# Optimization experiments

Hardware: AMD Instinct MI355X
Metric: run time of the kernel (lower is better)

The kernel has to match this reference:

```python
import jax, jax.numpy as jnp
import numpy as np

NUM_HEADS = 16
TEMPERATURE = 1.0


def setup_inputs() -> dict:
    key = jax.random.key(0)
    ks = jax.random.split(key, 6)
    B, H = 2048, 2048
    return {
        "hidden_states": jax.random.normal(ks[0], (B, H), dtype=jnp.float32),
        "attention_mask": jnp.ones((B,), dtype=bool),
        "Wq": jax.random.normal(ks[1], (H, H), dtype=jnp.float32) * 0.02,
        "Wk": jax.random.normal(ks[2], (H, H), dtype=jnp.float32) * 0.02,
        "Wv": jax.random.normal(ks[3], (H, H), dtype=jnp.float32) * 0.02,
        "Wo": jax.random.normal(ks[4], (H, H), dtype=jnp.float32) * 0.02,
        "scale_param": jnp.full((1,), -3.0, dtype=jnp.float32),
    }


def reference(hidden_states, attention_mask, Wq, Wk, Wv, Wo, scale_param):
    B, H = hidden_states.shape
    nh = NUM_HEADS
    hd = H // nh
    # projections (torch Linear: x @ W.T), reshape to [heads, batch, head_dim]
    q = (hidden_states @ Wq.T).reshape(B, nh, hd).transpose(1, 0, 2)
    k = (hidden_states @ Wk.T).reshape(B, nh, hd).transpose(1, 0, 2)
    v = (hidden_states @ Wv.T).reshape(B, nh, hd).transpose(1, 0, 2)
    # cross-batch scores [heads, B, B]
    scores = jnp.einsum('hqd,hkd->hqk', q, k) / (hd ** 0.5 * TEMPERATURE)
    neg_inf = jnp.float32(-jnp.inf)
    eye = jnp.eye(B, dtype=bool)  # exclude self-attention (diagonal)
    scores = jnp.where(eye[None, :, :], neg_inf, scores)
    scores = jnp.where(attention_mask[None, None, :], scores, neg_inf)
    attn = jax.nn.softmax(scores, axis=-1)
    attn = jnp.nan_to_num(attn, nan=0.0)  # rows fully masked -> 0 (dropout=0 is identity)
    ctx = jnp.einsum('hqk,hkd->hqd', attn, v)  # [heads, B, head_dim]
    ctx = ctx.transpose(1, 0, 2).reshape(B, H)
    cross = ctx @ Wo.T
    scale = jax.nn.sigmoid(scale_param[0])
    return hidden_states + scale * cross
```

## Files before the change

### kernel.cpp

```cpp
#include <hip/hip_runtime.h>

typedef __bf16 bf16;
typedef __attribute__((ext_vector_type(8))) __bf16 bf16x8;
typedef __attribute__((ext_vector_type(4))) float f32x4;
typedef __attribute__((ext_vector_type(4))) short s16x4;

#define HDIM 2048

__device__ __forceinline__ void glds16(const void* g, void* l) {
  __builtin_amdgcn_global_load_lds((const __attribute__((address_space(1))) void*)g,
                                   (__attribute__((address_space(3))) void*)l,
                                   16, 0, 0);
}

#define MFMA16(a, b, c) __builtin_amdgcn_mfma_f32_16x16x32_bf16(a, b, c, 0, 0, 0)

__global__ __launch_bounds__(256) void cvt5(
    const float* __restrict__ s0, const float* __restrict__ s1,
    const float* __restrict__ s2, const float* __restrict__ s3,
    const float* __restrict__ s4,
    bf16* __restrict__ d0, bf16* __restrict__ d1, bf16* __restrict__ d2,
    bf16* __restrict__ d3, bf16* __restrict__ d4) {
  const float* s; bf16* d;
  switch (blockIdx.y) {
    case 0: s = s0; d = d0; break;
    case 1: s = s1; d = d1; break;
    case 2: s = s2; d = d2; break;
    case 3: s = s3; d = d3; break;
    default: s = s4; d = d4; break;
  }
  const size_t base = (size_t)blockIdx.x * 4096 + (threadIdx.x << 2);
  for (int i = 0; i < 4; i++) {
    const float4 v = *(const float4*)(s + base + i * 1024);
    union { bf16 h[4]; s16x4 s4v; } u;
    u.h[0] = (bf16)v.x; u.h[1] = (bf16)v.y; u.h[2] = (bf16)v.z; u.h[3] = (bf16)v.w;
    *(s16x4*)(d + base + i * 1024) = u.s4v;
  }
}

__device__ __forceinline__ void gemm128_core(const bf16* __restrict__ A,
                                             const bf16* __restrict__ B,
                                             int rowBase, int colBase,
                                             f32x4 acc[4][4],
                                             bf16* ldsA, bf16* ldsB) {
  const int t = threadIdx.x;
  const int w = t >> 6, l = t & 63;
  const int wr = (w >> 1) << 6, wc = (w & 1) << 6;
  const int lr = l & 15, lq = l >> 4;

  for (int mi = 0; mi < 4; mi++)
    for (int ni = 0; ni < 4; ni++)
      for (int r = 0; r < 4; r++) acc[mi][ni][r] = 0.f;

  const int sRow = (w << 4) + (l >> 2);
  const int sCol = (l & 3) << 3;
  const bf16* gA = A + (size_t)(rowBase + sRow) * HDIM + sCol;
  const bf16* gB = B + (size_t)(colBase + sRow) * HDIM + sCol;
  bf16* lA = ldsA + (w << 9);
  bf16* lB = ldsB + (w << 9);

  for (int k0 = 0; k0 < HDIM; k0 += 32) {
    glds16(gA, lA);
    glds16(gA + (size_t)64 * HDIM, lA + 2048);
    glds16(gB, lB);
    glds16(gB + (size_t)64 * HDIM, lB + 2048);
    gA += 32; gB += 32;
    __syncthreads();

    bf16x8 af[4], bfr[4];
    for (int mi = 0; mi < 4; mi++)
      af[mi] = *(const bf16x8*)&ldsA[(wr + mi * 16 + lr) * 32 + lq * 8];
    for (int ni = 0; ni < 4; ni++)
      bfr[ni] = *(const bf16x8*)&ldsB[(wc + ni * 16 + lr) * 32 + lq * 8];
    for (int mi = 0; mi < 4; mi++)
      for (int ni = 0; ni < 4; ni++)
        acc[mi][ni] = MFMA16(af[mi], bfr[ni], acc[mi][ni]);
    __syncthreads();
  }
}

__global__ __launch_bounds__(256) void qkv_gemm(
    const bf16* __restrict__ hs, const bf16* __restrict__ Wq,
    const bf16* __restrict__ Wk, const bf16* __restrict__ Wv,
    bf16* __restrict__ qb, bf16* __restrict__ Kf, bf16* __restrict__ Vf) {
  __shared__ bf16 ldsA[128 * 32];
  __shared__ bf16 ldsB[128 * 32];
  const int z = blockIdx.z;
  const bf16* W = (z == 0) ? Wq : (z == 1) ? Wk : Wv;
  const int rowBase = blockIdx.y << 7, colBase = blockIdx.x << 7;
  f32x4 acc[4][4];
  gemm128_core(hs, W, rowBase, colBase, acc, ldsA, ldsB);

  const int t = threadIdx.x;
  const int w = t >> 6, l = t & 63;
  const int wr = (w >> 1) << 6, wc = (w & 1) << 6;
  const int lr = l & 15, lq = l >> 4;

  if (z == 0) {
    for (int mi = 0; mi < 4; mi++)
      for (int ni = 0; ni < 4; ni++) {
        const int col = colBase + wc + ni * 16 + lr;
        const int row0 = rowBase + wr + mi * 16 + lq * 4;
        for (int r = 0; r < 4; r++)
          qb[(size_t)(row0 + r) * HDIM + col] = (bf16)acc[mi][ni][r];
      }
  } else if (z == 1) {
    for (int mi = 0; mi < 4; mi++)
      for (int ni = 0; ni < 4; ni++) {
        const int dim = colBase + wc + ni * 16 + lr;
        const int hh = dim >> 7, ks = (dim >> 5) & 3, kh = (dim >> 3) & 3, j = dim & 7;
        const int row0 = rowBase + wr + mi * 16 + lq * 4;
        for (int r = 0; r < 4; r++) {
          const int key = row0 + r;
          const int kbk = key >> 7, kni = (key >> 4) & 7, kl = key & 15;
          Kf[(((size_t)hh * 16 + kbk) * 32 + kni * 4 + ks) * 512 +
             (kh * 16 + kl) * 8 + j] = (bf16)acc[mi][ni][r];
        }
      }
  } else {
    for (int mi = 0; mi < 4; mi++)
      for (int ni = 0; ni < 4; ni++) {
        const int dim = colBase + wc + ni * 16 + lr;
        const int hh = dim >> 7, vni = (dim >> 4) & 7, ll = dim & 15;
        const int row0 = rowBase + wr + mi * 16 + lq * 4;
        const int kbk = row0 >> 7, ks = (row0 >> 5) & 3, lh = (row0 >> 3) & 3;
        const int j0 = row0 & 7;
        union { bf16 h4[4]; s16x4 v; } u;
        for (int r = 0; r < 4; r++) u.h4[r] = (bf16)acc[mi][ni][r];
        *(s16x4*)&Vf[(((size_t)hh * 16 + kbk) * 32 + vni * 4 + ks) * 512 +
                     (lh * 16 + ll) * 8 + j0] = u.v;
      }
  }
}

__global__ __launch_bounds__(256, 2) void attn_kernel(
    const bf16* __restrict__ qb, const bf16* __restrict__ Kf,
    const bf16* __restrict__ Vf, const unsigned char* __restrict__ amask,
    bf16* __restrict__ ctx) {
  __shared__ bf16 Kl[32 * 512];
  __shared__ bf16 Vl[32 * 512];
  __shared__ bf16 Pl[4 * 16 * 128];

  const int qt = blockIdx.x, h = blockIdx.y;
  const int t = threadIdx.x, w = t >> 6, l = t & 63;
  const int lr = l & 15, lq = l >> 4;
  bf16* Pw = Pl + (w << 11);

  bf16x8 aq[4];
  for (int ks = 0; ks < 4; ks++)
    aq[ks] = *(const bf16x8*)&qb[(size_t)(qt * 64 + w * 16 + lr) * HDIM +
                                 h * 128 + ks * 32 + lq * 8];

  f32x4 o[8];
  for (int ni = 0; ni < 8; ni++)
    for (int r = 0; r < 4; r++) o[ni][r] = 0.f;
  float lsum[4] = {0.f, 0.f, 0.f, 0.f};
  int qrow[4];
  for (int r = 0; r < 4; r++) qrow[r] = qt * 64 + w * 16 + lq * 4 + r;

  const float c = 0.08838834764831845f * 1.4426950408889634f;

  for (int kbk = 0; kbk < 16; kbk++) {
    const size_t tileOff = ((size_t)h * 16 + kbk) * 32 * 512;

    for (int i = 0; i < 8; i++) {
      const int frag = i * 4 + w;
      glds16(Kf + tileOff + frag * 512 + l * 8, Kl + frag * 512);
    }
    bf16x8 vtmp[8];
    for (int i = 0; i < 8; i++) {
      const int frag = i * 4 + w;
      vtmp[i] = *(const bf16x8*)&Vf[tileOff + frag * 512 + l * 8];
    }
    for (int i = 0; i < 8; i++) {
      const int frag = i * 4 + w;
      *(bf16x8*)&Vl[frag * 512 + l * 8] = vtmp[i];
    }
    __syncthreads();

    f32x4 s[8];
    for (int ni = 0; ni < 8; ni++)
      for (int r = 0; r < 4; r++) s[ni][r] = 0.f;
    for (int ks = 0; ks < 4; ks++) {
      bf16x8 bk[8];
      for (int ni = 0; ni < 8; ni++)
        bk[ni] = *(const bf16x8*)&Kl[(ni * 4 + ks) * 512 + l * 8];
      for (int ni = 0; ni < 8; ni++) s[ni] = MFMA16(aq[ks], bk[ni], s[ni]);
    }

    float mk[8];
    for (int ni = 0; ni < 8; ni++)
      mk[ni] = amask[kbk * 128 + ni * 16 + lr] ? 1.f : 0.f;
    const bool diagBlk = (kbk == (qt >> 1));
    for (int ni = 0; ni < 8; ni++) {
      const int col = kbk * 128 + ni * 16 + lr;
      for (int r = 0; r < 4; r++) {
        float p = __builtin_exp2f(s[ni][r] * c) * mk[ni];
        if (diagBlk && col == qrow[r]) p = 0.f;
        s[ni][r] = p;
        lsum[r] += p;
      }
    }

    for (int ni = 0; ni < 8; ni++)
      for (int r = 0; r < 4; r++) {
        const int row = lq * 4 + r;
        Pw[row * 128 + (((ni * 2 + (lr >> 3)) ^ row) << 3) + (lr & 7)] = (bf16)s[ni][r];
      }

    for (int ks = 0; ks < 4; ks++) {
      bf16x8 bv[8];
      for (int ni = 0; ni < 8; ni++)
        bv[ni] = *(const bf16x8*)&Vl[(ni * 4 + ks) * 512 + l * 8];
      const bf16x8 ap = *(const bf16x8*)&Pw[lr * 128 + (((ks * 4 + lq) ^ lr) << 3)];
      for (int ni = 0; ni < 8; ni++) o[ni] = MFMA16(ap, bv[ni], o[ni]);
    }
    __syncthreads();
  }

  for (int r = 0; r < 4; r++)
    for (int off = 1; off < 16; off <<= 1)
      lsum[r] += __shfl_xor(lsum[r], off);

  for (int ni = 0; ni < 8; ni++)
    for (int r = 0; r < 4; r++) {
      const int row = qrow[r];
      const int col = h * 128 + ni * 16 + lr;
      const float li = lsum[r];
      ctx[(size_t)row * HDIM + col] = (bf16)((li > 0.f) ? o[ni][r] / li : 0.f);
    }
}

__global__ __launch_bounds__(256) void out_gemm(
    const bf16* __restrict__ ctx, const bf16* __restrict__ Wo,
    const float* __restrict__ hs, const float* __restrict__ scale_p,
    float* __restrict__ outp) {
  __shared__ bf16 ldsA[128 * 32];
  __shared__ bf16 ldsB[64 * 32];
  const int rowBase = blockIdx.y << 7, colBase = blockIdx.x << 6;
  const int t = threadIdx.x;
  const int w = t >> 6, l = t & 63;
  const int wr = (w >> 1) << 6, wc = (w & 1) << 5;
  const int lr = l & 15, lq = l >> 4;

  f32x4 acc[4][2];
  for (int mi = 0; mi < 4; mi++)
    for (int ni = 0; ni < 2; ni++)
      for (int r = 0; r < 4; r++) acc[mi][ni][r] = 0.f;

  const int sRow = (w << 4) + (l >> 2);
  const int sCol = (l & 3) << 3;
  const bf16* gA = ctx + (size_t)(rowBase + sRow) * HDIM + sCol;
  const bf16* gB = Wo + (size_t)(colBase + sRow) * HDIM + sCol;
  bf16* lA = ldsA + (w << 9);
  bf16* lB = ldsB + (w << 9);

  for (int k0 = 0; k0 < HDIM; k0 += 32) {
    glds16(gA, lA);
    glds16(gA + (size_t)64 * HDIM, lA + 2048);
    glds16(gB, lB);
    gA += 32; gB += 32;
    __syncthreads();

    bf16x8 af[4], bfr[2];
    for (int mi = 0; mi < 4; mi++)
      af[mi] = *(const bf16x8*)&ldsA[(wr + mi * 16 + lr) * 32 + lq * 8];
    for (int ni = 0; ni < 2; ni++)
      bfr[ni] = *(const bf16x8*)&ldsB[(wc + ni * 16 + lr) * 32 + lq * 8];
    for (int mi = 0; mi < 4; mi++)
      for (int ni = 0; ni < 2; ni++)
        acc[mi][ni] = MFMA16(af[mi], bfr[ni], acc[mi][ni]);
    __syncthreads();
  }

  const float sig = 1.0f / (1.0f + __expf(-scale_p[0]));
  for (int mi = 0; mi < 4; mi++)
    for (int ni = 0; ni < 2; ni++) {
      const int col = colBase + wc + ni * 16 + lr;
      const int row0 = rowBase + wr + mi * 16 + lq * 4;
      for (int r = 0; r < 4; r++) {
        const size_t idx = (size_t)(row0 + r) * HDIM + col;
        outp[idx] = hs[idx] + sig * acc[mi][ni][r];
      }
    }
}

extern "C" void kernel_launch(void* const* d_in, const int* in_sizes, int n_in,
                              void* d_out, int out_size, void* d_ws, size_t ws_size,
                              hipStream_t stream) {
  const float* hs = (const float*)d_in[0];
  const unsigned char* amask = (const unsigned char*)d_in[1];
  const float* Wq = (const float*)d_in[2];
  const float* Wk = (const float*)d_in[3];
  const float* Wv = (const float*)d_in[4];
  const float* Wo = (const float*)d_in[5];
  const float* scale_p = (const float*)d_in[6];
  float* outp = (float*)d_out;

  const size_t N = (size_t)HDIM * HDIM;
  bf16* qb   = (bf16*)d_ws;
  bf16* Kf   = qb + N;
  bf16* Vf   = Kf + N;
  bf16* ctx  = Vf + N;
  bf16* hs16 = ctx + N;
  bf16* Wq16 = hs16 + N;
  bf16* Wk16 = Wq16 + N;
  bf16* Wv16 = Wk16 + N;
  bf16* Wo16 = Wv16 + N;

  cvt5<<<dim3(1024, 5), 256, 0, stream>>>(hs, Wq, Wk, Wv, Wo,
                                          hs16, Wq16, Wk16, Wv16, Wo16);
  qkv_gemm<<<dim3(16, 16, 3), 256, 0, stream>>>(hs16, Wq16, Wk16, Wv16, qb, Kf, Vf);
  attn_kernel<<<dim3(32, 16), 256, 0, stream>>>(qb, Kf, Vf, amask, ctx);
  out_gemm<<<dim3(32, 16), 256, 0, stream>>>(ctx, Wo16, hs, scale_p, outp);
}
```

Measured before the change: 278.3 us.

## Split attention keys across waves and use fragment-ordered LDS tiles in GEMMs

The GEMM kernels now stage A/B tiles in LDS in MFMA-fragment order, so each lane reads one contiguous 16-byte chunk and the old row-strided reads that caused bank conflicts go away. The attention kernel reorganises its warps into 2 query groups × 2 key halves. Each wave handles 32 query rows against 64 keys, computing S transposed and reading the mask as a packed word. Partial outputs and row sums are combined through LDS at the end. This raises reuse of K/V fragments per wave, at the cost of an extra cross-wave reduction and the extra synchronisation it needs.

```diff
diff --git a/kernel.cpp b/kernel.cpp
--- a/kernel.cpp
+++ b/kernel.cpp
@@ -45,33 +45,36 @@
                                              bf16* ldsA, bf16* ldsB) {
   const int t = threadIdx.x;
   const int w = t >> 6, l = t & 63;
-  const int wr = (w >> 1) << 6, wc = (w & 1) << 6;
-  const int lr = l & 15, lq = l >> 4;
 
   for (int mi = 0; mi < 4; mi++)
     for (int ni = 0; ni < 4; ni++)
       for (int r = 0; r < 4; r++) acc[mi][ni][r] = 0.f;
 
-  const int sRow = (w << 4) + (l >> 2);
-  const int sCol = (l & 3) << 3;
-  const bf16* gA = A + (size_t)(rowBase + sRow) * HDIM + sCol;
-  const bf16* gB = B + (size_t)(colBase + sRow) * HDIM + sCol;
-  bf16* lA = ldsA + (w << 9);
-  bf16* lB = ldsB + (w << 9);
+  const int fr = l & 15;
+  const int fc = (l >> 4) << 3;
+  const bf16* gA0 = A + (size_t)(rowBase + w * 32 + fr) * HDIM + fc;
+  const bf16* gA1 = gA0 + (size_t)16 * HDIM;
+  const bf16* gB0 = B + (size_t)(colBase + w * 32 + fr) * HDIM + fc;
+  const bf16* gB1 = gB0 + (size_t)16 * HDIM;
+  bf16* lA = ldsA + (w << 10);
+  bf16* lB = ldsB + (w << 10);
+
+  const int af0 = (w >> 1) << 2;
+  const int bf0 = (w & 1) << 2;
 
   for (int k0 = 0; k0 < HDIM; k0 += 32) {
-    glds16(gA, lA);
-    glds16(gA + (size_t)64 * HDIM, lA + 2048);
-    glds16(gB, lB);
-    glds16(gB + (size_t)64 * HDIM, lB + 2048);
-    gA += 32; gB += 32;
+    glds16(gA0, lA);
+    glds16(gA1, lA + 512);
+    glds16(gB0, lB);
+    glds16(gB1, lB + 512);
+    gA0 += 32; gA1 += 32; gB0 += 32; gB1 += 32;
     __syncthreads();
 
     bf16x8 af[4], bfr[4];
     for (int mi = 0; mi < 4; mi++)
-      af[mi] = *(const bf16x8*)&ldsA[(wr + mi * 16 + lr) * 32 + lq * 8];
+      af[mi] = *(const bf16x8*)&ldsA[(af0 + mi) * 512 + l * 8];
     for (int ni = 0; ni < 4; ni++)
-      bfr[ni] = *(const bf16x8*)&ldsB[(wc + ni * 16 + lr) * 32 + lq * 8];
+      bfr[ni] = *(const bf16x8*)&ldsB[(bf0 + ni) * 512 + l * 8];
     for (int mi = 0; mi < 4; mi++)
       for (int ni = 0; ni < 4; ni++)
         acc[mi][ni] = MFMA16(af[mi], bfr[ni], acc[mi][ni]);
@@ -139,26 +142,28 @@
     bf16* __restrict__ ctx) {
   __shared__ bf16 Kl[32 * 512];
   __shared__ bf16 Vl[32 * 512];
-  __shared__ bf16 Pl[4 * 16 * 128];
+  __shared__ bf16 Pl[4 * 2048];
 
   const int qt = blockIdx.x, h = blockIdx.y;
   const int t = threadIdx.x, w = t >> 6, l = t & 63;
   const int lr = l & 15, lq = l >> 4;
+  const int wq = w & 1, wk = w >> 1;
   bf16* Pw = Pl + (w << 11);
 
-  bf16x8 aq[4];
-  for (int ks = 0; ks < 4; ks++)
-    aq[ks] = *(const bf16x8*)&qb[(size_t)(qt * 64 + w * 16 + lr) * HDIM +
-                                 h * 128 + ks * 32 + lq * 8];
-
-  f32x4 o[8];
-  for (int ni = 0; ni < 8; ni++)
-    for (int r = 0; r < 4; r++) o[ni][r] = 0.f;
-  float lsum[4] = {0.f, 0.f, 0.f, 0.f};
-  int qrow[4];
-  for (int r = 0; r < 4; r++) qrow[r] = qt * 64 + w * 16 + lq * 4 + r;
+  bf16x8 aq[2][4];
+  for (int mi = 0; mi < 2; mi++)
+    for (int ks = 0; ks < 4; ks++)
+      aq[mi][ks] = *(const bf16x8*)&qb[(size_t)(qt * 64 + wq * 32 + mi * 16 + lr) * HDIM +
+                                       h * 128 + ks * 32 + lq * 8];
+
+  f32x4 o[2][8];
+  for (int mi = 0; mi < 2; mi++)
+    for (int ni = 0; ni < 8; ni++)
+      for (int r = 0; r < 4; r++) o[mi][ni][r] = 0.f;
+  float lsum[2] = {0.f, 0.f};
 
   const float c = 0.08838834764831845f * 1.4426950408889634f;
+  const int lr7 = lr & 7;
 
   for (int kbk = 0; kbk < 16; kbk++) {
     const size_t tileOff = ((size_t)h * 16 + kbk) * 32 * 512;
@@ -168,67 +173,103 @@
       glds16(Kf + tileOff + frag * 512 + l * 8, Kl + frag * 512);
     }
     bf16x8 vtmp[8];
-    for (int i = 0; i < 8; i++) {
-      const int frag = i * 4 + w;
-      vtmp[i] = *(const bf16x8*)&Vf[tileOff + frag * 512 + l * 8];
-    }
-    for (int i = 0; i < 8; i++) {
-      const int frag = i * 4 + w;
-      *(bf16x8*)&Vl[frag * 512 + l * 8] = vtmp[i];
-    }
-    __syncthreads();
-
-    f32x4 s[8];
-    for (int ni = 0; ni < 8; ni++)
-      for (int r = 0; r < 4; r++) s[ni][r] = 0.f;
+    for (int i = 0; i < 8; i++)
+      vtmp[i] = *(const bf16x8*)&Vf[tileOff + (i * 4 + w) * 512 + l * 8];
+    for (int i = 0; i < 8; i++)
+      *(bf16x8*)&Vl[(i * 4 + w) * 512 + l * 8] = vtmp[i];
+    __syncthreads();
+
+    f32x4 s[2][4];
+    for (int mi = 0; mi < 2; mi++)
+      for (int ni = 0; ni < 4; ni++)
+        for (int r = 0; r < 4; r++) s[mi][ni][r] = 0.f;
     for (int ks = 0; ks < 4; ks++) {
-      bf16x8 bk[8];
-      for (int ni = 0; ni < 8; ni++)
-        bk[ni] = *(const bf16x8*)&Kl[(ni * 4 + ks) * 512 + l * 8];
-      for (int ni = 0; ni < 8; ni++) s[ni] = MFMA16(aq[ks], bk[ni], s[ni]);
-    }
-
-    float mk[8];
-    for (int ni = 0; ni < 8; ni++)
-      mk[ni] = amask[kbk * 128 + ni * 16 + lr] ? 1.f : 0.f;
-    const bool diagBlk = (kbk == (qt >> 1));
-    for (int ni = 0; ni < 8; ni++) {
-      const int col = kbk * 128 + ni * 16 + lr;
+      bf16x8 bk[4];
+      for (int ni = 0; ni < 4; ni++)
+        bk[ni] = *(const bf16x8*)&Kl[((wk * 4 + ni) * 4 + ks) * 512 + l * 8];
+      for (int mi = 0; mi < 2; mi++)
+        for (int ni = 0; ni < 4; ni++)
+          s[mi][ni] = MFMA16(bk[ni], aq[mi][ks], s[mi][ni]);
+    }
+
+    const bool dblk = (((kbk << 1) | wk) == qt);
+    for (int ni = 0; ni < 4; ni++) {
+      const int kbase = kbk * 128 + wk * 64 + ni * 16 + lq * 4;
+      const unsigned mword = *(const unsigned*)&amask[kbase];
+      for (int mi = 0; mi < 2; mi++) {
+        const int qrowg = qt * 64 + wq * 32 + mi * 16 + lr;
+        for (int r = 0; r < 4; r++) {
+          float p = __builtin_exp2f(s[mi][ni][r] * c);
+          if (!((mword >> (8 * r)) & 0xffu)) p = 0.f;
+          if (dblk && (kbase + r == qrowg)) p = 0.f;
+          s[mi][ni][r] = p;
+          lsum[mi] += p;
+        }
+      }
+    }
+
+    for (int mi = 0; mi < 2; mi++)
+      for (int ni = 0; ni < 4; ni++) {
+        union { bf16 h4[4]; s16x4 v; } u;
+        for (int r = 0; r < 4; r++) u.h4[r] = (bf16)s[mi][ni][r];
+        const int row = mi * 16 + lr;
+        const int g = ((ni * 2 + (lq >> 1)) ^ lr7);
+        *(s16x4*)&Pw[row * 64 + (g << 3) + ((lq & 1) << 2)] = u.v;
+      }
+
+    for (int ks2 = 0; ks2 < 2; ks2++) {
+      bf16x8 ap[2];
+      for (int mi = 0; mi < 2; mi++)
+        ap[mi] = *(const bf16x8*)&Pw[(mi * 16 + lr) * 64 +
+                                     (((ks2 * 4 + lq) ^ lr7) << 3)];
+      for (int ni = 0; ni < 8; ni++) {
+        const bf16x8 bv = *(const bf16x8*)&Vl[(ni * 4 + wk * 2 + ks2) * 512 + l * 8];
+        for (int mi = 0; mi < 2; mi++)
+          o[mi][ni] = MFMA16(ap[mi], bv, o[mi][ni]);
+      }
+    }
+    __syncthreads();
+  }
+
+  for (int mi = 0; mi < 2; mi++) {
+    lsum[mi] += __shfl_xor(lsum[mi], 16);
+    lsum[mi] += __shfl_xor(lsum[mi], 32);
+  }
+
+  float* Ocomb = (float*)Kl;
+  float* Ls = (float*)Vl;
+  if (wk == 1) {
+    f32x4* dst = (f32x4*)Ocomb + wq * 1024;
+    for (int i = 0; i < 16; i++) dst[i * 64 + l] = o[i >> 3][i & 7];
+    if (lq == 0) {
+      Ls[wq * 32 + lr] = lsum[0];
+      Ls[wq * 32 + 16 + lr] = lsum[1];
+    }
+  }
+  __syncthreads();
+  if (wk == 0) {
+    const f32x4* src = (const f32x4*)Ocomb + wq * 1024;
+    for (int i = 0; i < 16; i++) {
+      const f32x4 v = src[i * 64 + l];
+      for (int r = 0; r < 4; r++) o[i >> 3][i & 7][r] += v[r];
+    }
+    lsum[0] += Ls[wq * 32 + lr];
+    lsum[1] += Ls[wq * 32 + 16 + lr];
+    Ls[64 + wq * 32 + lr] = lsum[0];
+    Ls[64 + wq * 32 + 16 + lr] = lsum[1];
+  }
+  __syncthreads();
+  if (wk == 0) {
+    for (int mi = 0; mi < 2; mi++)
       for (int r = 0; r < 4; r++) {
-        float p = __builtin_exp2f(s[ni][r] * c) * mk[ni];
-        if (diagBlk && col == qrow[r]) p = 0.f;
-        s[ni][r] = p;
-        lsum[r] += p;
-      }
-    }
-
-    for (int ni = 0; ni < 8; ni++)
-      for (int r = 0; r < 4; r++) {
-        const int row = lq * 4 + r;
-        Pw[row * 128 + (((ni * 2 + (lr >> 3)) ^ row) << 3) + (lr & 7)] = (bf16)s[ni][r];
-      }
-
-    for (int ks = 0; ks < 4; ks++) {
-      bf16x8 bv[8];
-      for (int ni = 0; ni < 8; ni++)
-        bv[ni] = *(const bf16x8*)&Vl[(ni * 4 + ks) * 512 + l * 8];
-      const bf16x8 ap = *(const bf16x8*)&Pw[lr * 128 + (((ks * 4 + lq) ^ lr) << 3)];
-      for (int ni = 0; ni < 8; ni++) o[ni] = MFMA16(ap, bv[ni], o[ni]);
-    }
-    __syncthreads();
-  }
-
-  for (int r = 0; r < 4; r++)
-    for (int off = 1; off < 16; off <<= 1)
-      lsum[r] += __shfl_xor(lsum[r], off);
-
-  for (int ni = 0; ni < 8; ni++)
-    for (int r = 0; r < 4; r++) {
-      const int row = qrow[r];
-      const int col = h * 128 + ni * 16 + lr;
-      const float li = lsum[r];
-      ctx[(size_t)row * HDIM + col] = (bf16)((li > 0.f) ? o[ni][r] / li : 0.f);
-    }
+        const float li = Ls[64 + wq * 32 + mi * 16 + lq * 4 + r];
+        const int row = qt * 64 + wq * 32 + mi * 16 + lq * 4 + r;
+        for (int ni = 0; ni < 8; ni++) {
+          const float val = (li > 0.f) ? o[mi][ni][r] / li : 0.f;
+          ctx[(size_t)row * HDIM + h * 128 + ni * 16 + lr] = (bf16)val;
+        }
+      }
+  }
 }
 
 __global__ __launch_bounds__(256) void out_gemm(
@@ -248,25 +289,29 @@
     for (int ni = 0; ni < 2; ni++)
       for (int r = 0; r < 4; r++) acc[mi][ni][r] = 0.f;
 
-  const int sRow = (w << 4) + (l >> 2);
-  const int sCol = (l & 3) << 3;
-  const bf16* gA = ctx + (size_t)(rowBase + sRow) * HDIM + sCol;
-  const bf16* gB = Wo + (size_t)(colBase + sRow) * HDIM + sCol;
-  bf16* lA = ldsA + (w << 9);
+  const int fr = l & 15;
+  const int fc = (l >> 4) << 3;
+  const bf16* gA0 = ctx + (size_t)(rowBase + w * 32 + fr) * HDIM + fc;
+  const bf16* gA1 = gA0 + (size_t)16 * HDIM;
+  const bf16* gB0 = Wo + (size_t)(colBase + w * 16 + fr) * HDIM + fc;
+  bf16* lA = ldsA + (w << 10);
   bf16* lB = ldsB + (w << 9);
 
+  const int af0 = (w >> 1) << 2;
+  const int bf0 = (w & 1) << 1;
+
   for (int k0 = 0; k0 < HDIM; k0 += 32) {
-    glds16(gA, lA);
-    glds16(gA + (size_t)64 * HDIM, lA + 2048);
-    glds16(gB, lB);
-    gA += 32; gB += 32;
+    glds16(gA0, lA);
+    glds16(gA1, lA + 512);
+    glds16(gB0, lB);
+    gA0 += 32; gA1 += 32; gB0 += 32;
     __syncthreads();
 
     bf16x8 af[4], bfr[2];
     for (int mi = 0; mi < 4; mi++)
-      af[mi] = *(const bf16x8*)&ldsA[(wr + mi * 16 + lr) * 32 + lq * 8];
+      af[mi] = *(const bf16x8*)&ldsA[(af0 + mi) * 512 + l * 8];
     for (int ni = 0; ni < 2; ni++)
-      bfr[ni] = *(const bf16x8*)&ldsB[(wc + ni * 16 + lr) * 32 + lq * 8];
+      bfr[ni] = *(const bf16x8*)&ldsB[(bf0 + ni) * 512 + l * 8];
     for (int mi = 0; mi < 4; mi++)
       for (int ni = 0; ni < 2; ni++)
         acc[mi][ni] = MFMA16(af[mi], bfr[ni], acc[mi][ni]);
```

New measurement: 323.5 us. 1.16x slower.
